# Optimization experiments

Measured on AMD Instinct MI355X. Metric: run time of the kernel, lower is better.

Reference implementation:

```python
import jax, jax.numpy as jnp
import numpy as np

N_STATE = 1024
N_HEAD = 16
DIM_PER_HEAD = N_STATE // N_HEAD  # 64
QK_SCALE = DIM_PER_HEAD ** (-0.5)
B, T, T_CACHE = 8, 256, 768


def setup_inputs() -> dict:
    key = jax.random.key(0)
    ks = jax.random.split(key, 12)
    s = 0.02
    return {
        "x": jax.random.normal(ks[0], (B, T, N_STATE), dtype=jnp.float32),
        "qk_mask": jnp.zeros((T, T_CACHE + T), dtype=jnp.float32),
        "cache_k": jax.random.normal(ks[1], (B, T_CACHE, N_STATE), dtype=jnp.float32),
        "cache_v": jax.random.normal(ks[2], (B, T_CACHE, N_STATE), dtype=jnp.float32),
        "Wq": jax.random.normal(ks[3], (N_STATE, N_STATE), dtype=jnp.float32) * s,
        "bq": jax.random.normal(ks[4], (N_STATE,), dtype=jnp.float32) * s,
        "Wk": jax.random.normal(ks[5], (N_STATE, N_STATE), dtype=jnp.float32) * s,
        "Wv": jax.random.normal(ks[6], (N_STATE, N_STATE), dtype=jnp.float32) * s,
        "bv": jax.random.normal(ks[7], (N_STATE,), dtype=jnp.float32) * s,
        "Wo": jax.random.normal(ks[8], (N_STATE, N_STATE), dtype=jnp.float32) * s,
        "bo": jax.random.normal(ks[9], (N_STATE,), dtype=jnp.float32) * s,
    }


def reference(x, qk_mask, cache_k, cache_v, Wq, bq, Wk, Wv, bv, Wo, bo):
    # Linear projections (weights stored as [in, out], i.e. torch weight^T)
    q = (x @ Wq + bq) * QK_SCALE            # [B, T, D]
    new_k = x @ Wk                           # key has no bias
    new_v = x @ Wv + bv
    # KV-cache concat along time
    k = jnp.concatenate([cache_k, new_k], axis=1)  # [B, Tkv, D]
    v = jnp.concatenate([cache_v, new_v], axis=1)
    # Split heads
    Bq, Tq = q.shape[:2]
    Tkv = k.shape[1]
    qh = q.reshape(Bq, Tq, N_HEAD, DIM_PER_HEAD)    # [B, T, H, d]
    kh = k.reshape(Bq, Tkv, N_HEAD, DIM_PER_HEAD)
    vh = v.reshape(Bq, Tkv, N_HEAD, DIM_PER_HEAD)
    # q @ k^T + mask, softmax over keys
    qk = jnp.einsum("bthd,bshd->bhts", qh, kh) + qk_mask  # [B, H, T, Tkv]
    w = jax.nn.softmax(qk, axis=-1).astype(qh.dtype)
    wv = jnp.einsum("bhts,bshd->bthd", w, vh).reshape(Bq, Tq, N_STATE)
    out = wv @ Wo + bo
    return out, new_k, new_v
```

## Files before the change

### kernel.cpp

```cpp
#include <hip/hip_runtime.h>
#include <hip/hip_bf16.h>
#include <stdint.h>

#define Bb 8
#define Tt 256
#define TCC 768
#define TKV 1024
#define NS 1024
#define NH 16
#define DH 64
#define QK_SCALE 0.125f

typedef short bf16x8 __attribute__((ext_vector_type(8)));
typedef float f32x4 __attribute__((ext_vector_type(4)));
typedef unsigned int u32;

__device__ __forceinline__ unsigned short f2bf(float f) {
  union { float f; uint32_t u; } v; v.f = f;
  uint32_t u = v.u;
  u += 0x7fff + ((u >> 16) & 1);
  return (unsigned short)(u >> 16);
}

__device__ __forceinline__ void gload16(const unsigned short* g, unsigned short* l) {
  __builtin_amdgcn_global_load_lds(
      (__attribute__((address_space(1))) u32*)g,
      (__attribute__((address_space(3))) u32*)l,
      16, 0, 0);
}

__global__ __launch_bounds__(256) void convert_flat(
    const float* __restrict__ x, const float* __restrict__ ck,
    unsigned short* __restrict__ xb, unsigned short* __restrict__ kb) {
  const int64_t nx4 = (int64_t)Bb * Tt * NS / 4;
  const int64_t nk4 = (int64_t)Bb * TCC * NS / 4;
  int64_t stride = (int64_t)gridDim.x * blockDim.x;
  for (int64_t t = (int64_t)blockIdx.x * blockDim.x + threadIdx.x; t < nx4 + nk4; t += stride) {
    if (t < nx4) {
      float4 v = ((const float4*)x)[t];
      ushort4 o; o.x = f2bf(v.x); o.y = f2bf(v.y); o.z = f2bf(v.z); o.w = f2bf(v.w);
      ((ushort4*)xb)[t] = o;
    } else {
      int64_t e = t - nx4;
      float4 v = ((const float4*)ck)[e];
      ushort4 o; o.x = f2bf(v.x); o.y = f2bf(v.y); o.z = f2bf(v.z); o.w = f2bf(v.w);
      int64_t el = e * 4;
      int64_t b = el / ((int64_t)TCC * NS);
      int64_t rem = el % ((int64_t)TCC * NS);
      int64_t d = b * (int64_t)TKV * NS + rem;
      ((ushort4*)kb)[d / 4] = o;
    }
  }
}

__global__ __launch_bounds__(256) void transpose_convert(
    const float* __restrict__ Wq, const float* __restrict__ Wk,
    const float* __restrict__ Wv, const float* __restrict__ Wo,
    const float* __restrict__ cv,
    unsigned short* __restrict__ wqt, unsigned short* __restrict__ wkt,
    unsigned short* __restrict__ wvt, unsigned short* __restrict__ wot,
    unsigned short* __restrict__ vbt) {
  __shared__ float tile[64][65];
  int bid = blockIdx.x;
  const float* src; unsigned short* dst;
  if (bid < 1024) {
    int mat = bid >> 8, t = bid & 255;
    int tr = t >> 4, tc = t & 15;
    const float* W = (mat == 0) ? Wq : (mat == 1) ? Wk : (mat == 2) ? Wv : Wo;
    unsigned short* Wt = (mat == 0) ? wqt : (mat == 1) ? wkt : (mat == 2) ? wvt : wot;
    src = W + (int64_t)(tr * 64) * 1024 + tc * 64;
    dst = Wt + (int64_t)(tc * 64) * 1024 + tr * 64;
  } else {
    int e = bid - 1024;
    int b = e / 192; int t = e % 192;
    int st = t >> 4, ct = t & 15;
    src = cv + (int64_t)b * TCC * NS + (int64_t)(st * 64) * 1024 + ct * 64;
    dst = vbt + (int64_t)b * NS * TKV + (int64_t)(ct * 64) * 1024 + st * 64;
  }
  for (int e = threadIdx.x; e < 1024; e += 256) {
    int i = e >> 4, j4 = (e & 15) * 4;
    float4 v = *(const float4*)&src[(int64_t)i * 1024 + j4];
    tile[i][j4] = v.x; tile[i][j4 + 1] = v.y; tile[i][j4 + 2] = v.z; tile[i][j4 + 3] = v.w;
  }
  __syncthreads();
  for (int e = threadIdx.x; e < 1024; e += 256) {
    int i = e >> 4, j4 = (e & 15) * 4;
    ushort4 o;
    o.x = f2bf(tile[j4][i]); o.y = f2bf(tile[j4 + 1][i]);
    o.z = f2bf(tile[j4 + 2][i]); o.w = f2bf(tile[j4 + 3][i]);
    *(ushort4*)&dst[(int64_t)i * 1024 + j4] = o;
  }
}

template <int MODE>
__global__ __launch_bounds__(256) void gemm_mfma(
    const unsigned short* __restrict__ A,
    const unsigned short* __restrict__ Bt0, const unsigned short* __restrict__ Bt1,
    const unsigned short* __restrict__ Bt2,
    const float* __restrict__ bq, const float* __restrict__ bv,
    const float* __restrict__ bo,
    unsigned short* __restrict__ qb,
    float* __restrict__ okf, float* __restrict__ ovf,
    unsigned short* __restrict__ kb, unsigned short* __restrict__ vbt,
    float* __restrict__ outf) {
  constexpr int BM = 64;
  constexpr int BN = (MODE == 0) ? 128 : 64;
  constexpr int MT = 2;
  constexpr int NTf = BN / 32;
  __shared__ __align__(16) unsigned short As[2][BM * 64];
  __shared__ __align__(16) unsigned short Bs[2][BN * 64];

  int tid = threadIdx.x, lane = tid & 63, w = tid >> 6;
  int lr = lane & 15, hi = lane >> 4;
  int wm = w >> 1, wn = w & 1;

  int bid = blockIdx.x;
  int cpx = gridDim.x >> 3;
  int logical = (bid & 7) * cpx + (bid >> 3);

  int tm = logical & 31;
  int tn = logical >> 5;
  int seg, col0;
  const unsigned short* Bt;
  if (MODE == 0) {
    seg = tn >> 3; col0 = (tn & 7) * 128;
    Bt = (seg == 0) ? Bt0 : (seg == 1) ? Bt1 : Bt2;
  } else {
    seg = 0; col0 = tn * 64;
    Bt = Bt0;
  }
  int m0 = tm * 64;

  int srow = lane >> 3;
  int sch8 = (((lane & 7) ^ srow)) * 8;
  int sw = lr & 7;

  f32x4 acc[MT][NTf];
#pragma unroll
  for (int i = 0; i < MT; i++)
#pragma unroll
    for (int j = 0; j < NTf; j++) acc[i][j] = (f32x4){0.f, 0.f, 0.f, 0.f};

  auto STAGE = [&](int buf, int k0) {
#pragma unroll
    for (int i = 0; i < 2; i++) {
      int rb = w * 16 + i * 8;
      gload16(&A[(int64_t)(m0 + rb + srow) * 1024 + k0 + sch8], &As[buf][rb * 64]);
    }
#pragma unroll
    for (int i = 0; i < BN / 32; i++) {
      int rb = w * (BN / 4) + i * 8;
      gload16(&Bt[(int64_t)(col0 + rb + srow) * 1024 + k0 + sch8], &Bs[buf][rb * 64]);
    }
  };

  STAGE(0, 0);
  __syncthreads();
  int cur = 0;
  for (int step = 0; step < 16; ++step) {
    if (step < 15) STAGE(cur ^ 1, (step + 1) * 64);
    bf16x8 af[2][MT], bfr[2][NTf];
#pragma unroll
    for (int kk = 0; kk < 2; kk++) {
      int ch = ((kk * 4 + hi) ^ sw) * 8;
#pragma unroll
      for (int mt = 0; mt < MT; mt++)
        af[kk][mt] = *(const bf16x8*)&As[cur][(wm * 32 + mt * 16 + lr) * 64 + ch];
#pragma unroll
      for (int nt = 0; nt < NTf; nt++)
        bfr[kk][nt] = *(const bf16x8*)&Bs[cur][(wn * (BN / 2) + nt * 16 + lr) * 64 + ch];
    }
#pragma unroll
    for (int kk = 0; kk < 2; kk++)
#pragma unroll
      for (int mt = 0; mt < MT; mt++)
#pragma unroll
        for (int nt = 0; nt < NTf; nt++)
          acc[mt][nt] = __builtin_amdgcn_mfma_f32_16x16x32_bf16(af[kk][mt], bfr[kk][nt],
                                                               acc[mt][nt], 0, 0, 0);
    __syncthreads();
    cur ^= 1;
  }

#pragma unroll
  for (int mt = 0; mt < MT; mt++)
#pragma unroll
    for (int nt = 0; nt < NTf; nt++) {
      int row = m0 + wm * 32 + mt * 16 + hi * 4;
      int col = col0 + wn * (BN / 2) + nt * 16 + lr;
      if (MODE == 1) {
        float bias = bo[col];
#pragma unroll
        for (int r = 0; r < 4; r++)
          outf[(int64_t)(row + r) * 1024 + col] = acc[mt][nt][r] + bias;
      } else if (seg == 0) {
        float bias = bq[col];
#pragma unroll
        for (int r = 0; r < 4; r++)
          qb[(int64_t)(row + r) * 1024 + col] = f2bf((acc[mt][nt][r] + bias) * QK_SCALE);
      } else if (seg == 1) {
#pragma unroll
        for (int r = 0; r < 4; r++) {
          float v = acc[mt][nt][r];
          okf[(int64_t)(row + r) * 1024 + col] = v;
          int b = (row + r) >> 8, t = (row + r) & 255;
          kb[((int64_t)(b * TKV + TCC + t)) * 1024 + col] = f2bf(v);
        }
      } else {
        float bias = bv[col];
        int b = row >> 8, t0 = row & 255;
        int64_t voff = ((int64_t)(b * NH + (col >> 6)) * DH + (col & 63)) * TKV + TCC + t0;
        float v0 = acc[mt][nt][0] + bias, v1 = acc[mt][nt][1] + bias,
              v2 = acc[mt][nt][2] + bias, v3 = acc[mt][nt][3] + bias;
        ovf[(int64_t)(row + 0) * 1024 + col] = v0;
        ovf[(int64_t)(row + 1) * 1024 + col] = v1;
        ovf[(int64_t)(row + 2) * 1024 + col] = v2;
        ovf[(int64_t)(row + 3) * 1024 + col] = v3;
        ushort4 pk; pk.x = f2bf(v0); pk.y = f2bf(v1); pk.z = f2bf(v2); pk.w = f2bf(v3);
        *(ushort4*)&vbt[voff] = pk;
      }
    }
}

__global__ __launch_bounds__(256) void attn(
    const unsigned short* __restrict__ qb, const unsigned short* __restrict__ kb,
    const unsigned short* __restrict__ vbt, const float* __restrict__ mask,
    unsigned short* __restrict__ wvb) {
  __shared__ __align__(16) unsigned short Ks[2][64 * 64];
  __shared__ __align__(16) unsigned short Vs[2][64 * 64];
  __shared__ unsigned short Ps[4][16 * 76];

  int tid = threadIdx.x, lane = tid & 63, w = tid >> 6;
  int lr = lane & 15, hi = lane >> 4;
  int bid = blockIdx.x;
  int logical = (bid & 7) * 64 + (bid >> 3);
  int qt = logical & 3, bh = logical >> 2, b = bh >> 4, h = bh & 15;
  int q0 = qt * 64 + w * 16;

  const unsigned short* qp = qb + ((int64_t)(b * Tt + q0 + lr)) * 1024 + h * DH + hi * 8;
  bf16x8 aq0 = *(const bf16x8*)qp;
  bf16x8 aq1 = *(const bf16x8*)(qp + 32);

  f32x4 o[4];
#pragma unroll
  for (int nt = 0; nt < 4; nt++) o[nt] = (f32x4){0.f, 0.f, 0.f, 0.f};
  float m[4] = {-1e30f, -1e30f, -1e30f, -1e30f};
  float l[4] = {0.f, 0.f, 0.f, 0.f};

  const unsigned short* kbase = kb + (int64_t)b * TKV * 1024 + h * DH;
  const unsigned short* vbase = vbt + (int64_t)bh * DH * TKV;
  const float* mbase = mask + (int64_t)(q0 + hi * 4) * TKV;

  int srow = lane >> 3;
  int sch8 = ((lane & 7) ^ srow) * 8;
  int sw = lr & 7;

  auto STAGE = [&](int buf, int kv0) {
#pragma unroll
    for (int i = 0; i < 2; i++) {
      int rb = w * 16 + i * 8;
      gload16(&kbase[(int64_t)(kv0 + rb + srow) * 1024 + sch8], &Ks[buf][rb * 64]);
      gload16(&vbase[(int64_t)(rb + srow) * TKV + kv0 + sch8], &Vs[buf][rb * 64]);
    }
  };

  STAGE(0, 0);
  __syncthreads();
  int cur = 0;
  for (int c = 0; c < 16; ++c) {
    int kv0 = c * 64;
    if (c < 15) STAGE(cur ^ 1, kv0 + 64);

    float mk[4][4];
#pragma unroll
    for (int nt = 0; nt < 4; nt++)
#pragma unroll
      for (int r = 0; r < 4; r++)
        mk[nt][r] = mbase[(int64_t)r * TKV + kv0 + nt * 16 + lr];

    int ch0 = (hi ^ sw) * 8, ch1 = ((hi + 4) ^ sw) * 8;
    f32x4 s[4];
#pragma unroll
    for (int nt = 0; nt < 4; nt++) {
      int row = (nt * 16 + lr) * 64;
      bf16x8 bk0 = *(const bf16x8*)&Ks[cur][row + ch0];
      bf16x8 bk1 = *(const bf16x8*)&Ks[cur][row + ch1];
      f32x4 z = (f32x4){0.f, 0.f, 0.f, 0.f};
      z = __builtin_amdgcn_mfma_f32_16x16x32_bf16(aq0, bk0, z, 0, 0, 0);
      z = __builtin_amdgcn_mfma_f32_16x16x32_bf16(aq1, bk1, z, 0, 0, 0);
      s[nt] = z;
    }
#pragma unroll
    for (int nt = 0; nt < 4; nt++)
#pragma unroll
      for (int r = 0; r < 4; r++) s[nt][r] += mk[nt][r];

    float cm[4];
#pragma unroll
    for (int r = 0; r < 4; r++) {
      cm[r] = fmaxf(fmaxf(s[0][r], s[1][r]), fmaxf(s[2][r], s[3][r]));
#pragma unroll
      for (int d = 1; d < 16; d <<= 1) cm[r] = fmaxf(cm[r], __shfl_xor(cm[r], d));
    }
    float al[4], rs[4];
#pragma unroll
    for (int r = 0; r < 4; r++) {
      float nm = fmaxf(m[r], cm[r]);
      al[r] = __expf(m[r] - nm);
      m[r] = nm;
      rs[r] = 0.f;
    }
#pragma unroll
    for (int nt = 0; nt < 4; nt++)
#pragma unroll
      for (int r = 0; r < 4; r++) {
        s[nt][r] = __expf(s[nt][r] - m[r]);
        rs[r] += s[nt][r];
      }
#pragma unroll
    for (int r = 0; r < 4; r++) {
#pragma unroll
      for (int d = 1; d < 16; d <<= 1) rs[r] += __shfl_xor(rs[r], d);
      l[r] = l[r] * al[r] + rs[r];
    }
#pragma unroll
    for (int nt = 0; nt < 4; nt++)
#pragma unroll
      for (int r = 0; r < 4; r++) o[nt][r] *= al[r];

#pragma unroll
    for (int nt = 0; nt < 4; nt++)
#pragma unroll
      for (int r = 0; r < 4; r++)
        Ps[w][(hi * 4 + r) * 76 + nt * 16 + lr] = f2bf(s[nt][r]);
    bf16x8 pa0 = *(const bf16x8*)&Ps[w][lr * 76 + hi * 8];
    bf16x8 pa1 = *(const bf16x8*)&Ps[w][lr * 76 + 32 + hi * 8];

#pragma unroll
    for (int nt = 0; nt < 4; nt++) {
      int row = (nt * 16 + lr) * 64;
      bf16x8 bv0 = *(const bf16x8*)&Vs[cur][row + ch0];
      bf16x8 bv1 = *(const bf16x8*)&Vs[cur][row + ch1];
      o[nt] = __builtin_amdgcn_mfma_f32_16x16x32_bf16(pa0, bv0, o[nt], 0, 0, 0);
      o[nt] = __builtin_amdgcn_mfma_f32_16x16x32_bf16(pa1, bv1, o[nt], 0, 0, 0);
    }
    __syncthreads();
    cur ^= 1;
  }

  float inv[4];
#pragma unroll
  for (int r = 0; r < 4; r++) inv[r] = 1.f / l[r];
#pragma unroll
  for (int nt = 0; nt < 4; nt++)
#pragma unroll
    for (int r = 0; r < 4; r++)
      wvb[(int64_t)(b * Tt + q0 + hi * 4 + r) * 1024 + h * DH + nt * 16 + lr] =
          f2bf(o[nt][r] * inv[r]);
}

extern "C" void kernel_launch(void* const* d_in, const int* in_sizes, int n_in,
                              void* d_out, int out_size, void* d_ws, size_t ws_size,
                              hipStream_t stream) {
  const float* x    = (const float*)d_in[0];
  const float* mask = (const float*)d_in[1];
  const float* ck   = (const float*)d_in[2];
  const float* cv   = (const float*)d_in[3];
  const float* Wq   = (const float*)d_in[4];
  const float* bq   = (const float*)d_in[5];
  const float* Wk   = (const float*)d_in[6];
  const float* Wv   = (const float*)d_in[7];
  const float* bv   = (const float*)d_in[8];
  const float* Wo   = (const float*)d_in[9];
  const float* bo   = (const float*)d_in[10];

  const int64_t NT = (int64_t)Bb * Tt * NS;
  float* outp = (float*)d_out;
  float* okf  = outp + NT;
  float* ovf  = outp + 2 * NT;

  char* ws = (char*)d_ws;
  unsigned short* xb  = (unsigned short*)(ws);
  unsigned short* wqt = (unsigned short*)(ws + (4LL << 20));
  unsigned short* wkt = (unsigned short*)(ws + (6LL << 20));
  unsigned short* wvt = (unsigned short*)(ws + (8LL << 20));
  unsigned short* wot = (unsigned short*)(ws + (10LL << 20));
  unsigned short* qbw = (unsigned short*)(ws + (12LL << 20));
  unsigned short* kbw = (unsigned short*)(ws + (16LL << 20));
  unsigned short* vbt = (unsigned short*)(ws + (32LL << 20));
  unsigned short* wvb = (unsigned short*)(ws + (48LL << 20));

  convert_flat<<<2048, 256, 0, stream>>>(x, ck, xb, kbw);
  transpose_convert<<<2560, 256, 0, stream>>>(Wq, Wk, Wv, Wo, cv, wqt, wkt, wvt, wot, vbt);
  gemm_mfma<0><<<768, 256, 0, stream>>>(xb, wqt, wkt, wvt, bq, bv, bo,
                                        qbw, okf, ovf, kbw, vbt, outp);
  attn<<<512, 256, 0, stream>>>(qbw, kbw, vbt, mask, wvb);
  gemm_mfma<1><<<512, 256, 0, stream>>>(wvb, wot, wot, wot, bq, bv, bo,
                                        qbw, okf, ovf, kbw, vbt, outp);
}
```

Before: 211.5 us.

## Split attention KV range across two blocks with merge kernel, fuse prep kernels

```diff
diff --git a/kernel.cpp b/kernel.cpp
--- a/kernel.cpp
+++ b/kernel.cpp
@@ -29,61 +29,62 @@
       16, 0, 0);
 }
 
-__global__ __launch_bounds__(256) void convert_flat(
+__global__ __launch_bounds__(256) void prep(
     const float* __restrict__ x, const float* __restrict__ ck,
-    unsigned short* __restrict__ xb, unsigned short* __restrict__ kb) {
-  const int64_t nx4 = (int64_t)Bb * Tt * NS / 4;
-  const int64_t nk4 = (int64_t)Bb * TCC * NS / 4;
-  int64_t stride = (int64_t)gridDim.x * blockDim.x;
-  for (int64_t t = (int64_t)blockIdx.x * blockDim.x + threadIdx.x; t < nx4 + nk4; t += stride) {
-    if (t < nx4) {
-      float4 v = ((const float4*)x)[t];
-      ushort4 o; o.x = f2bf(v.x); o.y = f2bf(v.y); o.z = f2bf(v.z); o.w = f2bf(v.w);
-      ((ushort4*)xb)[t] = o;
-    } else {
-      int64_t e = t - nx4;
-      float4 v = ((const float4*)ck)[e];
-      ushort4 o; o.x = f2bf(v.x); o.y = f2bf(v.y); o.z = f2bf(v.z); o.w = f2bf(v.w);
-      int64_t el = e * 4;
-      int64_t b = el / ((int64_t)TCC * NS);
-      int64_t rem = el % ((int64_t)TCC * NS);
-      int64_t d = b * (int64_t)TKV * NS + rem;
-      ((ushort4*)kb)[d / 4] = o;
-    }
-  }
-}
-
-__global__ __launch_bounds__(256) void transpose_convert(
     const float* __restrict__ Wq, const float* __restrict__ Wk,
     const float* __restrict__ Wv, const float* __restrict__ Wo,
     const float* __restrict__ cv,
+    unsigned short* __restrict__ xb, unsigned short* __restrict__ kbw,
     unsigned short* __restrict__ wqt, unsigned short* __restrict__ wkt,
     unsigned short* __restrict__ wvt, unsigned short* __restrict__ wot,
     unsigned short* __restrict__ vbt) {
   __shared__ float tile[64][65];
-  int bid = blockIdx.x;
+  int bid = blockIdx.x, tid = threadIdx.x;
+  if (bid < 2048) {
+    const int64_t nx4 = (int64_t)Bb * Tt * NS / 4;
+    const int64_t nk4 = (int64_t)Bb * TCC * NS / 4;
+    const int64_t stride = 2048LL * 256;
+    for (int64_t t = (int64_t)bid * 256 + tid; t < nx4 + nk4; t += stride) {
+      if (t < nx4) {
+        float4 v = ((const float4*)x)[t];
+        ushort4 o; o.x = f2bf(v.x); o.y = f2bf(v.y); o.z = f2bf(v.z); o.w = f2bf(v.w);
+        ((ushort4*)xb)[t] = o;
+      } else {
+        int64_t e = t - nx4;
+        float4 v = ((const float4*)ck)[e];
+        ushort4 o; o.x = f2bf(v.x); o.y = f2bf(v.y); o.z = f2bf(v.z); o.w = f2bf(v.w);
+        int64_t el = e * 4;
+        int64_t b = el / ((int64_t)TCC * NS);
+        int64_t rem = el % ((int64_t)TCC * NS);
+        int64_t d = b * (int64_t)TKV * NS + rem;
+        ((ushort4*)kbw)[d / 4] = o;
+      }
+    }
+    return;
+  }
+  int tb = bid - 2048;
   const float* src; unsigned short* dst;
-  if (bid < 1024) {
-    int mat = bid >> 8, t = bid & 255;
+  if (tb < 1024) {
+    int mat = tb >> 8, t = tb & 255;
     int tr = t >> 4, tc = t & 15;
     const float* W = (mat == 0) ? Wq : (mat == 1) ? Wk : (mat == 2) ? Wv : Wo;
     unsigned short* Wt = (mat == 0) ? wqt : (mat == 1) ? wkt : (mat == 2) ? wvt : wot;
     src = W + (int64_t)(tr * 64) * 1024 + tc * 64;
     dst = Wt + (int64_t)(tc * 64) * 1024 + tr * 64;
   } else {
-    int e = bid - 1024;
+    int e = tb - 1024;
     int b = e / 192; int t = e % 192;
     int st = t >> 4, ct = t & 15;
     src = cv + (int64_t)b * TCC * NS + (int64_t)(st * 64) * 1024 + ct * 64;
     dst = vbt + (int64_t)b * NS * TKV + (int64_t)(ct * 64) * 1024 + st * 64;
   }
-  for (int e = threadIdx.x; e < 1024; e += 256) {
+  for (int e = tid; e < 1024; e += 256) {
     int i = e >> 4, j4 = (e & 15) * 4;
     float4 v = *(const float4*)&src[(int64_t)i * 1024 + j4];
     tile[i][j4] = v.x; tile[i][j4 + 1] = v.y; tile[i][j4 + 2] = v.z; tile[i][j4 + 3] = v.w;
   }
   __syncthreads();
-  for (int e = threadIdx.x; e < 1024; e += 256) {
+  for (int e = tid; e < 1024; e += 256) {
     int i = e >> 4, j4 = (e & 15) * 4;
     ushort4 o;
     o.x = f2bf(tile[j4][i]); o.y = f2bf(tile[j4 + 1][i]);
@@ -225,7 +226,7 @@
 __global__ __launch_bounds__(256) void attn(
     const unsigned short* __restrict__ qb, const unsigned short* __restrict__ kb,
     const unsigned short* __restrict__ vbt, const float* __restrict__ mask,
-    unsigned short* __restrict__ wvb) {
+    float* __restrict__ Op, float* __restrict__ Mp, float* __restrict__ Lp) {
   __shared__ __align__(16) unsigned short Ks[2][64 * 64];
   __shared__ __align__(16) unsigned short Vs[2][64 * 64];
   __shared__ unsigned short Ps[4][16 * 76];
@@ -233,9 +234,12 @@
   int tid = threadIdx.x, lane = tid & 63, w = tid >> 6;
   int lr = lane & 15, hi = lane >> 4;
   int bid = blockIdx.x;
-  int logical = (bid & 7) * 64 + (bid >> 3);
-  int qt = logical & 3, bh = logical >> 2, b = bh >> 4, h = bh & 15;
+  int logical = (bid & 7) * 128 + (bid >> 3);
+  int s = logical & 1;
+  int qt = (logical >> 1) & 3;
+  int bh = logical >> 3, b = bh >> 4, h = bh & 15;
   int q0 = qt * 64 + w * 16;
+  int kvbase = s * 512;
 
   const unsigned short* qp = qb + ((int64_t)(b * Tt + q0 + lr)) * 1024 + h * DH + hi * 8;
   bf16x8 aq0 = *(const bf16x8*)qp;
@@ -264,12 +268,12 @@
     }
   };
 
-  STAGE(0, 0);
+  STAGE(0, kvbase);
   __syncthreads();
   int cur = 0;
-  for (int c = 0; c < 16; ++c) {
-    int kv0 = c * 64;
-    if (c < 15) STAGE(cur ^ 1, kv0 + 64);
+  for (int c = 0; c < 8; ++c) {
+    int kv0 = kvbase + c * 64;
+    if (c < 7) STAGE(cur ^ 1, kv0 + 64);
 
     float mk[4][4];
 #pragma unroll
@@ -279,7 +283,7 @@
         mk[nt][r] = mbase[(int64_t)r * TKV + kv0 + nt * 16 + lr];
 
     int ch0 = (hi ^ sw) * 8, ch1 = ((hi + 4) ^ sw) * 8;
-    f32x4 s[4];
+    f32x4 sc[4];
 #pragma unroll
     for (int nt = 0; nt < 4; nt++) {
       int row = (nt * 16 + lr) * 64;
@@ -288,51 +292,49 @@
       f32x4 z = (f32x4){0.f, 0.f, 0.f, 0.f};
       z = __builtin_amdgcn_mfma_f32_16x16x32_bf16(aq0, bk0, z, 0, 0, 0);
       z = __builtin_amdgcn_mfma_f32_16x16x32_bf16(aq1, bk1, z, 0, 0, 0);
-      s[nt] = z;
+      sc[nt] = z;
     }
 #pragma unroll
     for (int nt = 0; nt < 4; nt++)
 #pragma unroll
-      for (int r = 0; r < 4; r++) s[nt][r] += mk[nt][r];
+      for (int r = 0; r < 4; r++) sc[nt][r] += mk[nt][r];
 
     float cm[4];
 #pragma unroll
     for (int r = 0; r < 4; r++) {
-      cm[r] = fmaxf(fmaxf(s[0][r], s[1][r]), fmaxf(s[2][r], s[3][r]));
+      cm[r] = fmaxf(fmaxf(sc[0][r], sc[1][r]), fmaxf(sc[2][r], sc[3][r]));
 #pragma unroll
       for (int d = 1; d < 16; d <<= 1) cm[r] = fmaxf(cm[r], __shfl_xor(cm[r], d));
     }
-    float al[4], rs[4];
 #pragma unroll
     for (int r = 0; r < 4; r++) {
-      float nm = fmaxf(m[r], cm[r]);
-      al[r] = __expf(m[r] - nm);
-      m[r] = nm;
-      rs[r] = 0.f;
-    }
+      if (cm[r] > m[r] + 8.f) {
+        float al = __expf(m[r] - cm[r]);
+        m[r] = cm[r];
+        l[r] *= al;
+        o[0][r] *= al; o[1][r] *= al; o[2][r] *= al; o[3][r] *= al;
+      }
+    }
+    float rs[4] = {0.f, 0.f, 0.f, 0.f};
 #pragma unroll
     for (int nt = 0; nt < 4; nt++)
 #pragma unroll
       for (int r = 0; r < 4; r++) {
-        s[nt][r] = __expf(s[nt][r] - m[r]);
-        rs[r] += s[nt][r];
+        sc[nt][r] = __expf(sc[nt][r] - m[r]);
+        rs[r] += sc[nt][r];
       }
 #pragma unroll
     for (int r = 0; r < 4; r++) {
 #pragma unroll
       for (int d = 1; d < 16; d <<= 1) rs[r] += __shfl_xor(rs[r], d);
-      l[r] = l[r] * al[r] + rs[r];
-    }
+      l[r] += rs[r];
+    }
+
 #pragma unroll
     for (int nt = 0; nt < 4; nt++)
 #pragma unroll
-      for (int r = 0; r < 4; r++) o[nt][r] *= al[r];
-
-#pragma unroll
-    for (int nt = 0; nt < 4; nt++)
-#pragma unroll
       for (int r = 0; r < 4; r++)
-        Ps[w][(hi * 4 + r) * 76 + nt * 16 + lr] = f2bf(s[nt][r]);
+        Ps[w][(hi * 4 + r) * 76 + nt * 16 + lr] = f2bf(sc[nt][r]);
     bf16x8 pa0 = *(const bf16x8*)&Ps[w][lr * 76 + hi * 8];
     bf16x8 pa1 = *(const bf16x8*)&Ps[w][lr * 76 + 32 + hi * 8];
 
@@ -348,15 +350,48 @@
     cur ^= 1;
   }
 
-  float inv[4];
-#pragma unroll
-  for (int r = 0; r < 4; r++) inv[r] = 1.f / l[r];
+  int p = (bh * 4 + qt) * 2 + s;
 #pragma unroll
   for (int nt = 0; nt < 4; nt++)
 #pragma unroll
-    for (int r = 0; r < 4; r++)
-      wvb[(int64_t)(b * Tt + q0 + hi * 4 + r) * 1024 + h * DH + nt * 16 + lr] =
-          f2bf(o[nt][r] * inv[r]);
+    for (int r = 0; r < 4; r++) {
+      int row = w * 16 + hi * 4 + r, col = nt * 16 + lr;
+      Op[(int64_t)p * 4096 + row * 64 + col] = o[nt][r];
+    }
+  if (lr == 0) {
+#pragma unroll
+    for (int r = 0; r < 4; r++) {
+      int row = w * 16 + hi * 4 + r;
+      Mp[p * 64 + row] = m[r];
+      Lp[p * 64 + row] = l[r];
+    }
+  }
+}
+
+__global__ __launch_bounds__(256) void attn_merge(
+    const float* __restrict__ Op, const float* __restrict__ Mp,
+    const float* __restrict__ Lp, unsigned short* __restrict__ wvb) {
+  int t = blockIdx.x * 256 + threadIdx.x;
+  int d4 = (t & 15) * 4;
+  int row = (t >> 4) & 63;
+  int pq = t >> 10;
+  int qt = pq & 3, bh = pq >> 2;
+  int b = bh >> 4, h = bh & 15;
+  int p0 = pq * 2, p1 = p0 + 1;
+  float m0 = Mp[p0 * 64 + row], m1 = Mp[p1 * 64 + row];
+  float l0 = Lp[p0 * 64 + row], l1 = Lp[p1 * 64 + row];
+  float M = fmaxf(m0, m1);
+  float w0 = __expf(m0 - M), w1 = __expf(m1 - M);
+  float inv = 1.f / (l0 * w0 + l1 * w1);
+  float4 o0 = *(const float4*)&Op[((int64_t)p0 * 64 + row) * 64 + d4];
+  float4 o1 = *(const float4*)&Op[((int64_t)p1 * 64 + row) * 64 + d4];
+  ushort4 pk;
+  pk.x = f2bf((o0.x * w0 + o1.x * w1) * inv);
+  pk.y = f2bf((o0.y * w0 + o1.y * w1) * inv);
+  pk.z = f2bf((o0.z * w0 + o1.z * w1) * inv);
+  pk.w = f2bf((o0.w * w0 + o1.w * w1) * inv);
+  int q = qt * 64 + row;
+  *(ushort4*)&wvb[(int64_t)(b * Tt + q) * 1024 + h * DH + d4] = pk;
 }
 
 extern "C" void kernel_launch(void* const* d_in, const int* in_sizes, int n_in,
@@ -389,12 +424,16 @@
   unsigned short* kbw = (unsigned short*)(ws + (16LL << 20));
   unsigned short* vbt = (unsigned short*)(ws + (32LL << 20));
   unsigned short* wvb = (unsigned short*)(ws + (48LL << 20));
-
-  convert_flat<<<2048, 256, 0, stream>>>(x, ck, xb, kbw);
-  transpose_convert<<<2560, 256, 0, stream>>>(Wq, Wk, Wv, Wo, cv, wqt, wkt, wvt, wot, vbt);
+  float* Op = (float*)(ws + (52LL << 20));
+  float* Mp = (float*)(ws + (68LL << 20));
+  float* Lp = (float*)(ws + (69LL << 20));
+
+  prep<<<4608, 256, 0, stream>>>(x, ck, Wq, Wk, Wv, Wo, cv,
+                                 xb, kbw, wqt, wkt, wvt, wot, vbt);
   gemm_mfma<0><<<768, 256, 0, stream>>>(xb, wqt, wkt, wvt, bq, bv, bo,
                                         qbw, okf, ovf, kbw, vbt, outp);
-  attn<<<512, 256, 0, stream>>>(qbw, kbw, vbt, mask, wvb);
+  attn<<<1024, 256, 0, stream>>>(qbw, kbw, vbt, mask, Op, Mp, Lp);
+  attn_merge<<<2048, 256, 0, stream>>>(Op, Mp, Lp, wvb);
   gemm_mfma<1><<<512, 256, 0, stream>>>(wvb, wot, wot, wot, bq, bv, bo,
                                         qbw, okf, ovf, kbw, vbt, outp);
 }
```

After: 214.1 us. About the same (+1.2%).
